# Kernel optimization log

Measured on AMD Instinct MI355X. Metric: run time of the kernel, lower is better.

The kernel has to match this reference:

```python
import jax, jax.numpy as jnp
import numpy as np

# irreps: 16x0e + 8x1o ; sh: 1x0e + 1x1o
M0, M1 = 16, 8
N_NODES, N_EDGES, N_BASIS = 10000, 160000, 8
DIM = M0 + 3 * M1                      # 40
NW = M0*M0 + M0*M1 + M1*M1 + M1*M0     # 576 per-edge TP weights
LOG2 = 0.6931471805599453


def _split(x):
    return x[:, :M0], x[:, M0:].reshape(-1, M1, 3)


def _merge(xs, xv):
    return jnp.concatenate([xs, xv.reshape(xv.shape[0], -1)], axis=1)


def _lin(x, Ws, Wv):
    # e3nn o3.Linear: per-irrep channel mixing, 1/sqrt(fan_in) path norm
    xs, xv = _split(x)
    return _merge(xs @ Ws / np.sqrt(M0),
                  jnp.einsum('nui,uv->nvi', xv, Wv) / np.sqrt(M1))


def _ssp(x):  # ShiftedSoftPlus
    return jax.nn.softplus(x) - LOG2


def setup_inputs() -> dict:
    key = jax.random.key(0)
    k = jax.random.split(key, 14)
    return {
        'x': jax.random.normal(k[0], (N_NODES, DIM), jnp.float32),
        'edge_radial': jax.random.uniform(k[1], (N_EDGES, N_BASIS), dtype=jnp.float32),
        'edge_sh': jax.random.normal(k[2], (N_EDGES, 4), jnp.float32),
        'edge_src': jax.random.randint(k[3], (N_EDGES,), 0, N_NODES),
        'edge_dst': jax.random.randint(k[4], (N_EDGES,), 0, N_NODES),
        'n_nodes': N_NODES,
        'W1s': jax.random.normal(k[5], (M0, M0), jnp.float32),
        'W1v': jax.random.normal(k[6], (M1, M1), jnp.float32),
        'Wfc': jax.random.normal(k[7], (N_BASIS, NW), jnp.float32),
        'W2s': jax.random.normal(k[8], (M0, M0), jnp.float32),
        'W2v': jax.random.normal(k[9], (M1, M1), jnp.float32),
        'R00': jax.random.normal(k[10], (M0, M0, M0), jnp.float32),
        'R01': jax.random.normal(k[11], (M0, M1, M1), jnp.float32),
        'R10': jax.random.normal(k[12], (M1, M0, M1), jnp.float32),
        'R11': jax.random.normal(k[13], (M1, M1, M0), jnp.float32),
    }


def reference(x, edge_radial, edge_sh, edge_src, edge_dst, n_nodes,
              W1s, W1v, Wfc, W2s, W2v, R00, R01, R10, R11):
    inv2 = 1.0 / np.sqrt(2.0)

    # linear_1
    h = _lin(x, W1s, W1v)
    hs, hv = _split(h)

    # SO3Convolution: per-edge TP weights from radial net
    sh0, sh1 = edge_sh[:, 0], edge_sh[:, 1:4]
    w = edge_radial @ Wfc / np.sqrt(N_BASIS)  # [E, NW]
    o = 0
    w00 = w[:, o:o + M0*M0].reshape(-1, M0, M0); o += M0*M0  # 0e x 0e -> 0e
    w01 = w[:, o:o + M0*M1].reshape(-1, M0, M1); o += M0*M1  # 0e x 1o -> 1o
    w10 = w[:, o:o + M1*M1].reshape(-1, M1, M1); o += M1*M1  # 1o x 0e -> 1o
    w11 = w[:, o:o + M1*M0].reshape(-1, M1, M0)              # 1o x 1o -> 0e (CG: delta/sqrt(3))

    xs_e, xv_e = hs[edge_src], hv[edge_src]  # gather
    msg_s = (jnp.einsum('eu,e,euw->ew', xs_e, sh0, w00) / np.sqrt(M0)
             + jnp.einsum('eui,ei,euw->ew', xv_e, sh1, w11) / np.sqrt(3.0 * M1)) * inv2
    msg_v = (jnp.einsum('eu,ei,euw->ewi', xs_e, sh1, w01) / np.sqrt(M0)
             + jnp.einsum('eui,e,euw->ewi', xv_e, sh0, w10) / np.sqrt(M1)) * inv2

    deg = np.sqrt(N_EDGES / N_NODES)
    outs = jax.ops.segment_sum(msg_s, edge_dst, num_segments=n_nodes) / deg
    outv = jax.ops.segment_sum(msg_v, edge_dst, num_segments=n_nodes) / deg

    # linear_2
    h = _lin(_merge(outs, outv), W2s, W2v)
    hs, hv = _split(h)

    # NormActivation (normalize=True, ShiftedSoftPlus, eps=1e-8)
    eps = 1e-8
    ns = jnp.sqrt(hs * hs + eps * eps)
    hs = hs / ns * _ssp(ns)
    nv = jnp.sqrt(jnp.sum(hv * hv, -1, keepdims=True) + eps * eps)
    hv = hv / nv * _ssp(nv)
    out = _merge(hs, hv)

    # residual FullyConnectedTensorProduct(x, x)
    xs, xv = _split(x)
    rs = (jnp.einsum('nu,nv,uvw->nw', xs, xs, R00) / M0
          + jnp.einsum('nui,nvi,uvw->nw', xv, xv, R11) / np.sqrt(3.0 * M1 * M1)) * inv2
    rv = (jnp.einsum('nu,nvi,uvw->nwi', xs, xv, R01) / np.sqrt(M0 * M1)
          + jnp.einsum('nui,nv,uvw->nwi', xv, xs, R10) / np.sqrt(M1 * M0)) * inv2

    return out + _merge(rs, rv)
```

## Files before the change

### kernel.cpp

```cpp
#include <hip/hip_runtime.h>
#include <math.h>

constexpr int kM0 = 16, kM1 = 8, kDim = 40, kNW = 576;
constexpr int kNodes = 10000, kEdges = 160000;
constexpr int kCap = 96;
constexpr int kNB = 24;

__device__ __forceinline__ float sspf(float x){
  float ax = fabsf(x);
  return fmaxf(x, 0.f) + log1pf(expf(-ax)) - 0.69314718055994531f;
}

__global__ void __launch_bounds__(256) k_pre(
    const float* __restrict__ x, const float* __restrict__ W1s,
    const float* __restrict__ W1v, const float* __restrict__ Wfc,
    const int* __restrict__ edst,
    float* __restrict__ h, float* __restrict__ WfcT,
    int* __restrict__ cnt, int* __restrict__ posw){
  int t = blockIdx.x*256 + threadIdx.x;
  posw[t] = atomicAdd(&cnt[edst[t]], 1);
  if (t < kNW){
    #pragma unroll
    for (int b=0;b<8;++b) WfcT[t*8+b] = Wfc[b*kNW + t];
  }
  if (t < kNodes){
    const float4* xp4 = (const float4*)(x + (size_t)t*kDim);
    float xx[40];
    #pragma unroll
    for (int i=0;i<10;++i){
      float4 v = xp4[i];
      xx[i*4]=v.x; xx[i*4+1]=v.y; xx[i*4+2]=v.z; xx[i*4+3]=v.w;
    }
    float hh[40];
    #pragma unroll
    for (int v=0; v<kM0; ++v){
      float acc = 0.f;
      #pragma unroll
      for (int u=0; u<kM0; ++u) acc += xx[u]*W1s[u*kM0+v];
      hh[v] = acc*0.25f;
    }
    #pragma unroll
    for (int v=0; v<kM1; ++v){
      float a0=0.f,a1=0.f,a2=0.f;
      #pragma unroll
      for (int u=0; u<kM1; ++u){
        float wv = W1v[u*kM1+v];
        a0 += xx[16+u*3+0]*wv;
        a1 += xx[16+u*3+1]*wv;
        a2 += xx[16+u*3+2]*wv;
      }
      hh[16+v*3+0]=a0*0.35355339059327373f;
      hh[16+v*3+1]=a1*0.35355339059327373f;
      hh[16+v*3+2]=a2*0.35355339059327373f;
    }
    float4* hp4 = (float4*)(h + (size_t)t*kDim);
    #pragma unroll
    for (int i=0;i<10;++i)
      hp4[i] = make_float4(hh[i*4],hh[i*4+1],hh[i*4+2],hh[i*4+3]);
  }
}

__global__ void __launch_bounds__(512) k_edge(
    const float* __restrict__ er, const float* __restrict__ esh,
    const int* __restrict__ esrc, const int* __restrict__ edst,
    const int* __restrict__ posw,
    const float* __restrict__ h, const float* __restrict__ WfcT,
    float* __restrict__ msg){
  int lane = threadIdx.x & 63;
  int q = __builtin_amdgcn_readfirstlane(threadIdx.x >> 6);
  int e = blockIdx.x*64 + lane;
  float4 ra = *(const float4*)(er + (size_t)e*8);
  float4 rb = *(const float4*)(er + (size_t)e*8 + 4);
  const float r0=ra.x,r1=ra.y,r2=ra.z,r3=ra.w,r4=rb.x,r5=rb.y,r6=rb.z,r7=rb.w;
  float4 s4 = *(const float4*)(esh + (size_t)e*4);
  const float* hp = h + (size_t)esrc[e]*kDim;
  float* mp = msg + ((size_t)edst[e]*kCap + posw[e])*kDim;

#define DOT8(p) ((p)[0]*r0+(p)[1]*r1+(p)[2]*r2+(p)[3]*r3+(p)[4]*r4+(p)[5]*r5+(p)[6]*r6+(p)[7]*r7)

  const int w0 = q*2;
  float t00a=0.f, t00b=0.f, t11a=0.f, t11b=0.f;
  float t01=0.f, tx=0.f, ty=0.f, tz=0.f;

  #pragma unroll
  for (int u=0;u<16;++u){
    float xu = hp[u];
    const float* p0 = WfcT + (size_t)(u*16 + w0)*8;
    t00a += xu*DOT8(p0);
    t00b += xu*DOT8(p0 + 8);
    const float* p1 = WfcT + (size_t)(256 + u*8 + q)*8;
    t01 += xu*DOT8(p1);
  }
  #pragma unroll
  for (int u=0;u<8;++u){
    float v0=hp[16+u*3], v1=hp[16+u*3+1], v2=hp[16+u*3+2];
    float au = v0*s4.y + v1*s4.z + v2*s4.w;
    const float* p3 = WfcT + (size_t)(448 + u*16 + w0)*8;
    t11a += au*DOT8(p3);
    t11b += au*DOT8(p3 + 8);
    const float* p2 = WfcT + (size_t)(384 + u*8 + q)*8;
    float a = DOT8(p2);
    tx += v0*a; ty += v1*a; tz += v2*a;
  }
#undef DOT8

  constexpr float cs00 = 0.0625f;
  constexpr float cs11 = 0.05103103630798288f;
  constexpr float cv01 = 0.0625f;
  constexpr float cv10 = 0.08838834764831845f;

  *(float2*)(mp + w0) = make_float2(s4.x*t00a*cs00 + t11a*cs11,
                                    s4.x*t00b*cs00 + t11b*cs11);
  float va = t01*cv01, sc0 = s4.x*cv10;
  float* vp = mp + 16 + q*3;
  vp[0] = s4.y*va + tx*sc0;
  vp[1] = s4.z*va + ty*sc0;
  vp[2] = s4.w*va + tz*sc0;
}

__global__ void __launch_bounds__(960) k_node(
    const float* __restrict__ x, const float* __restrict__ msg,
    const int* __restrict__ cnt,
    const float* __restrict__ W2s, const float* __restrict__ W2v,
    const float* __restrict__ R00, const float* __restrict__ R01,
    const float* __restrict__ R10, const float* __restrict__ R11,
    float* __restrict__ out){
  __shared__ float sR00[4096], sR01[1024], sR10[1024], sR11[1024];
  __shared__ float sW2s[256], sW2v[64];
  __shared__ float sx[kNB][40], sa[kNB][40];
  int t = threadIdx.x;
  for (int i=t; i<1024; i+=960) ((float4*)sR00)[i] = ((const float4*)R00)[i];
  if (t < 256){
    ((float4*)sR01)[t] = ((const float4*)R01)[t];
    ((float4*)sR10)[t] = ((const float4*)R10)[t];
    ((float4*)sR11)[t] = ((const float4*)R11)[t];
  }
  if (t < 64) ((float4*)sW2s)[t] = ((const float4*)W2s)[t];
  if (t < 16) ((float4*)sW2v)[t] = ((const float4*)W2v)[t];
  int nb = blockIdx.x*kNB;
  {
    int ns = t/40, c = t - ns*40, n = nb + ns;
    float a0=0.f,a1=0.f,a2=0.f,a3=0.f, xval=0.f;
    if (n < kNodes){
      int deg = cnt[n];
      const float* bp = msg + (size_t)n*kCap*kDim + c;
      int k=0;
      for (; k+4<=deg; k+=4){
        a0 += bp[(size_t)(k+0)*kDim];
        a1 += bp[(size_t)(k+1)*kDim];
        a2 += bp[(size_t)(k+2)*kDim];
        a3 += bp[(size_t)(k+3)*kDim];
      }
      for (; k<deg; ++k) a0 += bp[(size_t)k*kDim];
      xval = x[(size_t)n*kDim + c];
    }
    sa[ns][c] = ((a0+a1)+(a2+a3))*0.25f;
    sx[ns][c] = xval;
  }
  __syncthreads();
  if (t < kNB*16){
    int ns = t>>4, w = t&15, n = nb+ns;
    const float* ap = sa[ns];
    const float* xp = sx[ns];
    float hsum = 0.f;
    #pragma unroll
    for (int u=0;u<16;++u) hsum += ap[u]*sW2s[u*16+w];
    hsum *= 0.25f;
    float nrm = sqrtf(hsum*hsum + 1e-16f);
    float val = hsum/nrm*sspf(nrm);
    float xs[16];
    #pragma unroll
    for (int v=0;v<16;++v) xs[v] = xp[v];
    float r0 = 0.f;
    #pragma unroll
    for (int u=0;u<16;++u){
      float tacc = 0.f;
      #pragma unroll
      for (int v=0;v<16;++v) tacc += xs[v]*sR00[(u*16+v)*16+w];
      r0 += xs[u]*tacc;
    }
    float xv[24];
    #pragma unroll
    for (int c2=0;c2<24;++c2) xv[c2] = xp[16+c2];
    float r1 = 0.f;
    #pragma unroll
    for (int u=0;u<8;++u){
      #pragma unroll
      for (int v=0;v<8;++v){
        float dot = xv[u*3]*xv[v*3] + xv[u*3+1]*xv[v*3+1] + xv[u*3+2]*xv[v*3+2];
        r1 += dot*sR11[(u*8+v)*16+w];
      }
    }
    if (n < kNodes)
      out[(size_t)n*kDim + w] = val + 0.04419417382415922f*r0 + 0.05103103630798288f*r1;
  } else {
    int t2 = t - kNB*16;
    int ns = t2/24, cc = t2 - ns*24, w = cc/3, i = cc - w*3, n = nb+ns;
    const float* ap = sa[ns] + 16;
    const float* xp = sx[ns];
    float h0=0.f,h1=0.f,h2=0.f;
    #pragma unroll
    for (int u=0;u<8;++u){
      float wv = sW2v[u*8+w];
      h0 += ap[u*3+0]*wv; h1 += ap[u*3+1]*wv; h2 += ap[u*3+2]*wv;
    }
    const float sc = 0.35355339059327373f;
    h0*=sc; h1*=sc; h2*=sc;
    float nv = sqrtf(h0*h0+h1*h1+h2*h2 + 1e-16f);
    float hi = (i==0)?h0:((i==1)?h1:h2);
    float val = hi/nv*sspf(nv);
    float xs[16];
    #pragma unroll
    for (int v=0;v<16;++v) xs[v] = xp[v];
    float xvi[8];
    #pragma unroll
    for (int v=0;v<8;++v) xvi[v] = xp[16+v*3+i];
    float racc = 0.f;
    #pragma unroll
    for (int u=0;u<16;++u){
      float tacc=0.f;
      #pragma unroll
      for (int v=0;v<8;++v) tacc += xvi[v]*sR01[(u*8+v)*8+w];
      racc += xs[u]*tacc;
    }
    #pragma unroll
    for (int u=0;u<8;++u){
      float tacc=0.f;
      #pragma unroll
      for (int v=0;v<16;++v) tacc += xs[v]*sR10[(u*16+v)*8+w];
      racc += xvi[u]*tacc;
    }
    if (n < kNodes)
      out[(size_t)n*kDim + 16 + cc] = val + 0.0625f*racc;
  }
}

extern "C" void kernel_launch(void* const* d_in, const int* in_sizes, int n_in,
                              void* d_out, int out_size, void* d_ws, size_t ws_size,
                              hipStream_t stream){
  const float* x   = (const float*)d_in[0];
  const float* er  = (const float*)d_in[1];
  const float* esh = (const float*)d_in[2];
  const int*   esrc= (const int*)d_in[3];
  const int*   edst= (const int*)d_in[4];
  const float* W1s = (const float*)d_in[6];
  const float* W1v = (const float*)d_in[7];
  const float* Wfc = (const float*)d_in[8];
  const float* W2s = (const float*)d_in[9];
  const float* W2v = (const float*)d_in[10];
  const float* R00 = (const float*)d_in[11];
  const float* R01 = (const float*)d_in[12];
  const float* R10 = (const float*)d_in[13];
  const float* R11 = (const float*)d_in[14];
  float* out = (float*)d_out;

  char* wsb = (char*)d_ws;
  float* h    = (float*)wsb;
  float* msg  = h + (size_t)kNodes*kDim;
  float* WfcT = msg + (size_t)kNodes*kCap*kDim;
  int*   cnt  = (int*)(WfcT + (size_t)kNW*8);
  int*   posw = cnt + kNodes;

  hipMemsetAsync(cnt, 0, kNodes*sizeof(int), stream);
  k_pre<<<kEdges/256, 256, 0, stream>>>(x, W1s, W1v, Wfc, edst, h, WfcT, cnt, posw);
  k_edge<<<kEdges/64, 512, 0, stream>>>(er, esh, esrc, edst, posw, h, WfcT, msg);
  k_node<<<(kNodes+kNB-1)/kNB, 960, 0, stream>>>(x, msg, cnt, W2s, W2v, R00, R01, R10, R11, out);
}
```

Measured before the change: 158.5 us.

## Stage gathered source features in LDS and vectorize node-side message reduction

The edge kernel now cooperatively gathers each block's 64 source-node feature rows into shared memory with float4 loads. Each of the 8 waves then reads from LDS instead of repeating the same scalar global gather. In the node kernel, message slots are summed with float4 loads split across four k-phases, combined through a shared reduction buffer in an extra sync stage, and x is loaded as float4. This is meant to cut redundant and poorly coalesced global loads, at the cost of more LDS use, an extra barrier and reassigned loader threads.

After: 155.1 us. 2.2% less time.

```diff
diff --git a/kernel.cpp b/kernel.cpp
--- a/kernel.cpp
+++ b/kernel.cpp
@@ -66,14 +66,26 @@
     const int* __restrict__ posw,
     const float* __restrict__ h, const float* __restrict__ WfcT,
     float* __restrict__ msg){
-  int lane = threadIdx.x & 63;
-  int q = __builtin_amdgcn_readfirstlane(threadIdx.x >> 6);
-  int e = blockIdx.x*64 + lane;
+  __shared__ float sh_h[64][41];
+  int t = threadIdx.x;
+  int e0 = blockIdx.x*64;
+  for (int idx = t; idx < 640; idx += 512){
+    int el = idx/10, c4 = idx - el*10;
+    int src = esrc[e0 + el];
+    const float4 v = *(const float4*)(h + (size_t)src*kDim + c4*4);
+    float* d = &sh_h[el][c4*4];
+    d[0]=v.x; d[1]=v.y; d[2]=v.z; d[3]=v.w;
+  }
+  __syncthreads();
+
+  int lane = t & 63;
+  int q = __builtin_amdgcn_readfirstlane(t >> 6);
+  int e = e0 + lane;
   float4 ra = *(const float4*)(er + (size_t)e*8);
   float4 rb = *(const float4*)(er + (size_t)e*8 + 4);
   const float r0=ra.x,r1=ra.y,r2=ra.z,r3=ra.w,r4=rb.x,r5=rb.y,r6=rb.z,r7=rb.w;
   float4 s4 = *(const float4*)(esh + (size_t)e*4);
-  const float* hp = h + (size_t)esrc[e]*kDim;
+  const float* hl = sh_h[lane];
   float* mp = msg + ((size_t)edst[e]*kCap + posw[e])*kDim;
 
 #define DOT8(p) ((p)[0]*r0+(p)[1]*r1+(p)[2]*r2+(p)[3]*r3+(p)[4]*r4+(p)[5]*r5+(p)[6]*r6+(p)[7]*r7)
@@ -84,7 +96,7 @@
 
   #pragma unroll
   for (int u=0;u<16;++u){
-    float xu = hp[u];
+    float xu = hl[u];
     const float* p0 = WfcT + (size_t)(u*16 + w0)*8;
     t00a += xu*DOT8(p0);
     t00b += xu*DOT8(p0 + 8);
@@ -93,7 +105,7 @@
   }
   #pragma unroll
   for (int u=0;u<8;++u){
-    float v0=hp[16+u*3], v1=hp[16+u*3+1], v2=hp[16+u*3+2];
+    float v0=hl[16+u*3], v1=hl[16+u*3+1], v2=hl[16+u*3+2];
     float au = v0*s4.y + v1*s4.z + v2*s4.w;
     const float* p3 = WfcT + (size_t)(448 + u*16 + w0)*8;
     t11a += au*DOT8(p3);
@@ -128,6 +140,7 @@
   __shared__ float sR00[4096], sR01[1024], sR10[1024], sR11[1024];
   __shared__ float sW2s[256], sW2v[64];
   __shared__ float sx[kNB][40], sa[kNB][40];
+  __shared__ float4 sred[kNB][4][10];
   int t = threadIdx.x;
   for (int i=t; i<1024; i+=960) ((float4*)sR00)[i] = ((const float4*)R00)[i];
   if (t < 256){
@@ -135,27 +148,35 @@
     ((float4*)sR10)[t] = ((const float4*)R10)[t];
     ((float4*)sR11)[t] = ((const float4*)R11)[t];
   }
-  if (t < 64) ((float4*)sW2s)[t] = ((const float4*)W2s)[t];
-  if (t < 16) ((float4*)sW2v)[t] = ((const float4*)W2v)[t];
+  if (t >= 256 && t < 320) ((float4*)sW2s)[t-256] = ((const float4*)W2s)[t-256];
+  if (t >= 320 && t < 336) ((float4*)sW2v)[t-320] = ((const float4*)W2v)[t-320];
   int nb = blockIdx.x*kNB;
   {
-    int ns = t/40, c = t - ns*40, n = nb + ns;
-    float a0=0.f,a1=0.f,a2=0.f,a3=0.f, xval=0.f;
+    int ns = t/40; int rem = t - ns*40; int kq = rem/10; int c4 = rem - kq*10;
+    int n = nb + ns;
+    float4 acc = make_float4(0.f,0.f,0.f,0.f);
     if (n < kNodes){
       int deg = cnt[n];
-      const float* bp = msg + (size_t)n*kCap*kDim + c;
-      int k=0;
-      for (; k+4<=deg; k+=4){
-        a0 += bp[(size_t)(k+0)*kDim];
-        a1 += bp[(size_t)(k+1)*kDim];
-        a2 += bp[(size_t)(k+2)*kDim];
-        a3 += bp[(size_t)(k+3)*kDim];
+      const float* bp = msg + (size_t)n*kCap*kDim + c4*4;
+      for (int k=kq; k<deg; k+=4){
+        const float4 v = *(const float4*)(bp + (size_t)k*kDim);
+        acc.x+=v.x; acc.y+=v.y; acc.z+=v.z; acc.w+=v.w;
       }
-      for (; k<deg; ++k) a0 += bp[(size_t)k*kDim];
-      xval = x[(size_t)n*kDim + c];
-    }
-    sa[ns][c] = ((a0+a1)+(a2+a3))*0.25f;
-    sx[ns][c] = xval;
+    }
+    sred[ns][kq][c4] = acc;
+  }
+  __syncthreads();
+  if (t < kNB*10){
+    int ns = t/10, c4 = t - ns*10, n = nb+ns;
+    float4 a0 = sred[ns][0][c4], a1 = sred[ns][1][c4];
+    float4 a2 = sred[ns][2][c4], a3 = sred[ns][3][c4];
+    sa[ns][c4*4+0] = (a0.x+a1.x+a2.x+a3.x)*0.25f;
+    sa[ns][c4*4+1] = (a0.y+a1.y+a2.y+a3.y)*0.25f;
+    sa[ns][c4*4+2] = (a0.z+a1.z+a2.z+a3.z)*0.25f;
+    sa[ns][c4*4+3] = (a0.w+a1.w+a2.w+a3.w)*0.25f;
+    float4 xv = (n < kNodes) ? *(const float4*)(x + (size_t)n*kDim + c4*4)
+                             : make_float4(0.f,0.f,0.f,0.f);
+    sx[ns][c4*4+0]=xv.x; sx[ns][c4*4+1]=xv.y; sx[ns][c4*4+2]=xv.z; sx[ns][c4*4+3]=xv.w;
   }
   __syncthreads();
   if (t < kNB*16){
@@ -193,7 +214,7 @@
     }
     if (n < kNodes)
       out[(size_t)n*kDim + w] = val + 0.04419417382415922f*r0 + 0.05103103630798288f*r1;
-  } else {
+  } else if (t >= kNB*16 && t < kNB*16 + kNB*24) {
     int t2 = t - kNB*16;
     int ns = t2/24, cc = t2 - ns*24, w = cc/3, i = cc - w*3, n = nb+ns;
     const float* ap = sa[ns] + 16;
```
